# Performance work log

Measured on AMD Instinct MI355X. Metric: run time of the kernel, lower is better.

## Reference

```python
import jax, jax.numpy as jnp
import numpy as np

D_MODEL = 1024
NUM_HEADS = 16
THETA = 10000.0
B, T = 2, 2048


def _rope(x, pos, theta_base):
    # x: (b, h, t, d_h); interleaved pairs (x0,x1),(x2,x3),... per the
    # rearrange '... (c d) -> ... c d' with d=2 in the original module.
    d = x.shape[-1]
    half = d // 2
    inv_freq = 1.0 / (theta_base ** (2.0 * jnp.arange(half, dtype=jnp.float32) / d))
    ang = pos.astype(jnp.float32)[:, None] * inv_freq[None, :]  # (t, half)
    sin = jnp.sin(ang)[None, None]  # (1,1,t,half)
    cos = jnp.cos(ang)[None, None]
    x1 = x[..., 0::2]
    x2 = x[..., 1::2]
    r1 = x1 * cos - x2 * sin
    r2 = x1 * sin + x2 * cos
    return jnp.stack([r1, r2], axis=-1).reshape(x.shape)


def setup_inputs() -> dict:
    key = jax.random.key(0)
    k0, k1, k2, k3, k4 = jax.random.split(key, 5)
    sigma = (2.0 / (D_MODEL + D_MODEL)) ** 0.5
    return {
        "in_features": jax.random.normal(k0, (B, T, D_MODEL), dtype=jnp.float32),
        "Wq": jax.random.normal(k1, (D_MODEL, D_MODEL), dtype=jnp.float32) * sigma,
        "Wk": jax.random.normal(k2, (D_MODEL, D_MODEL), dtype=jnp.float32) * sigma,
        "Wv": jax.random.normal(k3, (D_MODEL, D_MODEL), dtype=jnp.float32) * sigma,
        "Wo": jax.random.normal(k4, (D_MODEL, D_MODEL), dtype=jnp.float32) * sigma,
        "token_positions": jnp.arange(T, dtype=jnp.int32),
    }


def reference(in_features, Wq, Wk, Wv, Wo, token_positions):
    b, t, d_model = in_features.shape
    h = NUM_HEADS
    d_h = d_model // h
    # Fused-style QKV projections (x @ W.T, weights stored (in, out))
    q = in_features @ Wq.T
    k = in_features @ Wk.T
    v = in_features @ Wv.T
    # (b, t, h*d_h) -> (b, h, t, d_h)
    q = q.reshape(b, t, h, d_h).transpose(0, 2, 1, 3)
    k = k.reshape(b, t, h, d_h).transpose(0, 2, 1, 3)
    v = v.reshape(b, t, h, d_h).transpose(0, 2, 1, 3)
    q = _rope(q, token_positions, THETA)
    k = _rope(k, token_positions, THETA)
    scale = 1.0 / jnp.sqrt(jnp.asarray(d_h, dtype=q.dtype))
    scores = jnp.einsum('bhqd,bhkd->bhqk', q, k) * scale
    causal = jnp.tril(jnp.ones((t, t), dtype=bool))
    scores = jnp.where(causal[None, None], scores, -jnp.inf)
    attn = jax.nn.softmax(scores, axis=-1)
    out = jnp.einsum('bhqk,bhkd->bhqd', attn, v)
    out = out.transpose(0, 2, 1, 3).reshape(b, t, h * d_h)
    return out @ Wo.T
```

## Files before the change

kernel.cpp:

```cpp
#include <hip/hip_runtime.h>

#define D_MODEL 1024
#define NUM_HEADS 16
#define DH 64
#define B_SZ 2
#define T_SZ 2048
#define M_ROWS (B_SZ * T_SZ)

typedef __bf16 bf16;
typedef __bf16 bf16x4 __attribute__((ext_vector_type(4)));
typedef __bf16 bf16x8 __attribute__((ext_vector_type(8)));
typedef float f32x4 __attribute__((ext_vector_type(4)));

__device__ __forceinline__ void async_copy16(const bf16* g, bf16* l) {
  __builtin_amdgcn_global_load_lds(
      (const __attribute__((address_space(1))) void*)g,
      (__attribute__((address_space(3))) void*)l, 16, 0, 0);
}

#define NX (M_ROWS * D_MODEL / 4)
#define NW (D_MODEL * D_MODEL / 4)

__global__ __launch_bounds__(256) void cast_all(
    const float* __restrict__ X, const float* __restrict__ Wq,
    const float* __restrict__ Wk, const float* __restrict__ Wv,
    const float* __restrict__ Wo,
    bf16* __restrict__ Xb, bf16* __restrict__ Wqb, bf16* __restrict__ Wkb,
    bf16* __restrict__ Wvb, bf16* __restrict__ Wob) {
  int i = blockIdx.x * 256 + threadIdx.x;
  const float* s; bf16* d; int off;
  if (i < NX) {
    s = X; d = Xb; off = i;
  } else {
    int j = i - NX;
    int w = j >> 18;
    off = j & (NW - 1);
    if (w == 0)      { s = Wq; d = Wqb; }
    else if (w == 1) { s = Wk; d = Wkb; }
    else if (w == 2) { s = Wv; d = Wvb; }
    else             { s = Wo; d = Wob; }
  }
  float4 v = ((const float4*)s)[off];
  bf16x4 o;
  o[0] = (bf16)v.x; o[1] = (bf16)v.y; o[2] = (bf16)v.z; o[3] = (bf16)v.w;
  ((bf16x4*)d)[off] = o;
}

__global__ __launch_bounds__(256) void qkv_gemm(
    const bf16* __restrict__ Xb,
    const bf16* __restrict__ Wqb, const bf16* __restrict__ Wkb,
    const bf16* __restrict__ Wvb,
    bf16* __restrict__ Q, bf16* __restrict__ K, bf16* __restrict__ V) {
  __shared__ bf16 As[128 * 32];
  __shared__ bf16 Bs[128 * 32];

  int tid = threadIdx.x;
  int wave = tid >> 6, lane = tid & 63;
  int wm = wave >> 1, wn = wave & 1;
  int l15 = lane & 15, quad = lane >> 4;

  int row0 = blockIdx.x * 128;
  int col0 = blockIdx.y * 128;
  int sel = col0 >> 10;
  int nb = col0 & 1023;
  const bf16* W; bf16* Out;
  if (sel == 0)      { W = Wqb; Out = Q; }
  else if (sel == 1) { W = Wkb; Out = K; }
  else               { W = Wvb; Out = V; }

  int srow = tid >> 2;
  int schunk = tid & 3;
  const bf16* Ag = Xb + (size_t)(row0 + srow) * D_MODEL + schunk * 8;
  const bf16* Bg = W + (size_t)(nb + srow) * D_MODEL + schunk * 8;
  bf16* Al0 = &As[srow * 32 + schunk * 8];
  bf16* Al1 = &As[(srow + 64) * 32 + schunk * 8];
  bf16* Bl0 = &Bs[srow * 32 + schunk * 8];
  bf16* Bl1 = &Bs[(srow + 64) * 32 + schunk * 8];

  f32x4 acc[4][4];
#pragma unroll
  for (int i = 0; i < 4; ++i)
#pragma unroll
    for (int j = 0; j < 4; ++j) acc[i][j] = (f32x4){0.f, 0.f, 0.f, 0.f};

  for (int k0 = 0; k0 < D_MODEL; k0 += 32) {
    async_copy16(Ag + k0, Al0);
    async_copy16(Ag + k0 + (size_t)64 * D_MODEL, Al1);
    async_copy16(Bg + k0, Bl0);
    async_copy16(Bg + k0 + (size_t)64 * D_MODEL, Bl1);
    __syncthreads();

    bf16x8 af[4], bfr[4];
#pragma unroll
    for (int i = 0; i < 4; ++i)
      af[i] = *(const bf16x8*)&As[(wm * 64 + i * 16 + l15) * 32 + quad * 8];
#pragma unroll
    for (int j = 0; j < 4; ++j)
      bfr[j] = *(const bf16x8*)&Bs[(wn * 64 + j * 16 + l15) * 32 + quad * 8];
#pragma unroll
    for (int i = 0; i < 4; ++i)
#pragma unroll
      for (int j = 0; j < 4; ++j)
        acc[i][j] = __builtin_amdgcn_mfma_f32_16x16x32_bf16(af[i], bfr[j],
                                                            acc[i][j], 0, 0, 0);
    __syncthreads();
  }

#pragma unroll
  for (int i = 0; i < 4; ++i) {
    int row = row0 + wm * 64 + i * 16 + quad * 4;
#pragma unroll
    for (int j = 0; j < 4; ++j) {
      int col = nb + wn * 64 + j * 16 + l15;
#pragma unroll
      for (int r = 0; r < 4; ++r)
        Out[(size_t)(row + r) * D_MODEL + col] = (bf16)acc[i][j][r];
    }
  }
}

#define ROPEK_BLOCKS (M_ROWS * NUM_HEADS * 32 / 256)

__global__ __launch_bounds__(256) void ropek_vt(
    bf16* __restrict__ K, const bf16* __restrict__ V, bf16* __restrict__ VT,
    const int* __restrict__ pos) {
  int b0 = blockIdx.x;
  if (b0 < ROPEK_BLOCKS) {
    int idx = b0 * 256 + threadIdx.x;
    int i = idx & 31;
    int h = (idx >> 5) & 15;
    int row = idx >> 9;
    int t = row & (T_SZ - 1);
    float p = (float)pos[t];
    float freq = __expf(-(float)i * 0.28782313662425f);
    float s, c;
    sincosf(p * freq, &s, &c);
    size_t base = (size_t)row * D_MODEL + h * DH + 2 * i;
    float k1 = (float)K[base], k2 = (float)K[base + 1];
    K[base]     = (bf16)(k1 * c - k2 * s);
    K[base + 1] = (bf16)(k1 * s + k2 * c);
  } else {
    __shared__ bf16 tile[64][72];
    int vb = b0 - ROPEK_BLOCKS;
    int bh = vb >> 5;
    int tt = vb & 31;
    int b = bh >> 4, h = bh & 15;
    int tid = threadIdx.x;
    int rr = tid >> 3;
    int cc = (tid & 7) * 8;
#pragma unroll
    for (int p = 0; p < 2; ++p) {
      int t = rr + p * 32;
      bf16x8 v = *(const bf16x8*)&V[((size_t)b * T_SZ + tt * 64 + t) * D_MODEL +
                                    h * DH + cc];
      *(bf16x8*)&tile[t][cc] = v;
    }
    __syncthreads();
#pragma unroll
    for (int p = 0; p < 2; ++p) {
      int d = rr + p * 32;
      bf16x8 o;
#pragma unroll
      for (int j = 0; j < 8; ++j) o[j] = tile[cc + j][d];
      *(bf16x8*)&VT[((size_t)bh * DH + d) * T_SZ + tt * 64 + cc] = o;
    }
  }
}

#define PST 72
#define KST 72

__global__ __launch_bounds__(256) void attn_kernel(
    const bf16* __restrict__ Q, const bf16* __restrict__ K,
    const bf16* __restrict__ VT, const int* __restrict__ pos,
    bf16* __restrict__ AO) {
  __shared__ bf16 Kt[64 * KST];
  __shared__ bf16 Vt[64 * KST];
  __shared__ bf16 Pbuf[4][16 * PST];

  int bh = blockIdx.x;
  int qi = 31 - (int)blockIdx.y;
  int bb = bh >> 4, h = bh & 15;
  int tid = threadIdx.x;
  int wave = tid >> 6, lane = tid & 63;
  int l15 = lane & 15, quad = lane >> 4;

  int q0 = qi * 64 + wave * 16;
  size_t grow = (size_t)bb * T_SZ + q0;

  const bf16* Qp = Q + (grow + l15) * D_MODEL + h * DH + quad * 8;
  bf16x8 bq0 = *(const bf16x8*)(Qp);
  bf16x8 bq1 = *(const bf16x8*)(Qp + 32);
  {
    float p = (float)pos[q0 + l15];
#pragma unroll
    for (int jj = 0; jj < 4; ++jj) {
      int i0 = quad * 4 + jj;
      float s, c;
      sincosf(p * __expf(-(float)i0 * 0.28782313662425f), &s, &c);
      float x1 = (float)bq0[2 * jj], x2 = (float)bq0[2 * jj + 1];
      bq0[2 * jj]     = (bf16)(x1 * c - x2 * s);
      bq0[2 * jj + 1] = (bf16)(x1 * s + x2 * c);
      sincosf(p * __expf(-(float)(i0 + 16) * 0.28782313662425f), &s, &c);
      float y1 = (float)bq1[2 * jj], y2 = (float)bq1[2 * jj + 1];
      bq1[2 * jj]     = (bf16)(y1 * c - y2 * s);
      bq1[2 * jj + 1] = (bf16)(y1 * s + y2 * c);
    }
  }

  f32x4 o[4];
#pragma unroll
  for (int nt = 0; nt < 4; ++nt) o[nt] = (f32x4){0.f, 0.f, 0.f, 0.f};
  float l_i = 0.f;

  int srow = tid >> 2;
  int sc = (tid & 3) * 16;
  const bf16* Kg = K + ((size_t)bb * T_SZ + srow) * D_MODEL + h * DH + sc;
  const bf16* Vg = VT + ((size_t)bh * DH + srow) * T_SZ + sc;
  bf16* Kl = &Kt[srow * KST + sc];
  bf16* Vl = &Vt[srow * KST + sc];

  bf16* Pw = Pbuf[wave];
  int nchunks = qi + 1;
  int rel = wave * 16 + l15;

  bf16x8 kr0 = *(const bf16x8*)(Kg);
  bf16x8 kr1 = *(const bf16x8*)(Kg + 8);
  bf16x8 vr0 = *(const bf16x8*)(Vg);
  bf16x8 vr1 = *(const bf16x8*)(Vg + 8);

  for (int t = 0; t < nchunks; ++t) {
    __syncthreads();
    *(bf16x8*)(Kl) = kr0;
    *(bf16x8*)(Kl + 8) = kr1;
    *(bf16x8*)(Vl) = vr0;
    *(bf16x8*)(Vl + 8) = vr1;
    if (t + 1 < nchunks) {
      const bf16* Kn = Kg + (size_t)(t + 1) * 64 * D_MODEL;
      const bf16* Vn = Vg + (t + 1) * 64;
      kr0 = *(const bf16x8*)(Kn);
      kr1 = *(const bf16x8*)(Kn + 8);
      vr0 = *(const bf16x8*)(Vn);
      vr1 = *(const bf16x8*)(Vn + 8);
    }
    __syncthreads();

    f32x4 st[4];
#pragma unroll
    for (int cs = 0; cs < 4; ++cs) {
      bf16x8 ak0 = *(const bf16x8*)&Kt[(cs * 16 + l15) * KST + quad * 8];
      bf16x8 ak1 = *(const bf16x8*)&Kt[(cs * 16 + l15) * KST + 32 + quad * 8];
      f32x4 s4 = (f32x4){0.f, 0.f, 0.f, 0.f};
      s4 = __builtin_amdgcn_mfma_f32_16x16x32_bf16(ak0, bq0, s4, 0, 0, 0);
      s4 = __builtin_amdgcn_mfma_f32_16x16x32_bf16(ak1, bq1, s4, 0, 0, 0);
      st[cs] = s4;
    }

    bool last = (t == nchunks - 1);
    float ps = 0.f;
#pragma unroll
    for (int cs = 0; cs < 4; ++cs)
#pragma unroll
      for (int r = 0; r < 4; ++r) {
        float p = __expf(st[cs][r] * 0.125f);
        if (last) {
          int cl = cs * 16 + quad * 4 + r;
          p = (cl > rel) ? 0.f : p;
        }
        st[cs][r] = p;
        ps += p;
      }
    l_i += ps;

#pragma unroll
    for (int cs = 0; cs < 4; ++cs) {
      bf16x4 pk;
#pragma unroll
      for (int r = 0; r < 4; ++r) pk[r] = (bf16)st[cs][r];
      *(bf16x4*)&Pw[l15 * PST + cs * 16 + quad * 4] = pk;
    }
    __asm__ __volatile__("" ::: "memory");
    bf16x8 bp0 = *(const bf16x8*)&Pw[l15 * PST + quad * 8];
    bf16x8 bp1 = *(const bf16x8*)&Pw[l15 * PST + 32 + quad * 8];
    __asm__ __volatile__("" ::: "memory");

#pragma unroll
    for (int nt = 0; nt < 4; ++nt) {
      bf16x8 av0 = *(const bf16x8*)&Vt[(nt * 16 + l15) * KST + quad * 8];
      bf16x8 av1 = *(const bf16x8*)&Vt[(nt * 16 + l15) * KST + 32 + quad * 8];
      o[nt] = __builtin_amdgcn_mfma_f32_16x16x32_bf16(av0, bp0, o[nt], 0, 0, 0);
      o[nt] = __builtin_amdgcn_mfma_f32_16x16x32_bf16(av1, bp1, o[nt], 0, 0, 0);
    }
  }

  l_i += __shfl_xor(l_i, 16);
  l_i += __shfl_xor(l_i, 32);
  float inv = 1.0f / l_i;
#pragma unroll
  for (int nt = 0; nt < 4; ++nt) {
    bf16x4 ov;
#pragma unroll
    for (int r = 0; r < 4; ++r) ov[r] = (bf16)(o[nt][r] * inv);
    *(bf16x4*)&AO[(grow + l15) * D_MODEL + h * DH + nt * 16 + quad * 4] = ov;
  }
}

__global__ __launch_bounds__(256) void out_gemm(
    const bf16* __restrict__ AO, const bf16* __restrict__ Wob,
    float* __restrict__ out) {
  __shared__ bf16 As[128 * 32];
  __shared__ bf16 Bs[64 * 32];

  int tid = threadIdx.x;
  int wave = tid >> 6, lane = tid & 63;
  int l15 = lane & 15, quad = lane >> 4;

  int row0 = blockIdx.x * 128;
  int nb = blockIdx.y * 64;

  int srow = tid >> 2;
  int schunk = tid & 3;
  const bf16* Ag = AO + (size_t)(row0 + srow) * D_MODEL + schunk * 8;
  const bf16* Bg = Wob + (size_t)(nb + srow) * D_MODEL + schunk * 8;
  bf16* Al0 = &As[srow * 32 + schunk * 8];
  bf16* Al1 = &As[(srow + 64) * 32 + schunk * 8];
  bf16* Bl = &Bs[srow * 32 + schunk * 8];

  f32x4 acc[2][4];
#pragma unroll
  for (int i = 0; i < 2; ++i)
#pragma unroll
    for (int j = 0; j < 4; ++j) acc[i][j] = (f32x4){0.f, 0.f, 0.f, 0.f};

  for (int k0 = 0; k0 < D_MODEL; k0 += 32) {
    async_copy16(Ag + k0, Al0);
    async_copy16(Ag + k0 + (size_t)64 * D_MODEL, Al1);
    async_copy16(Bg + k0, Bl);
    __syncthreads();

    bf16x8 af[2], bfr[4];
#pragma unroll
    for (int i = 0; i < 2; ++i)
      af[i] = *(const bf16x8*)&As[(wave * 32 + i * 16 + l15) * 32 + quad * 8];
#pragma unroll
    for (int j = 0; j < 4; ++j)
      bfr[j] = *(const bf16x8*)&Bs[(j * 16 + l15) * 32 + quad * 8];
#pragma unroll
    for (int i = 0; i < 2; ++i)
#pragma unroll
      for (int j = 0; j < 4; ++j)
        acc[i][j] = __builtin_amdgcn_mfma_f32_16x16x32_bf16(af[i], bfr[j],
                                                            acc[i][j], 0, 0, 0);
    __syncthreads();
  }

#pragma unroll
  for (int i = 0; i < 2; ++i) {
    int row = row0 + wave * 32 + i * 16 + quad * 4;
#pragma unroll
    for (int j = 0; j < 4; ++j) {
      int col = nb + j * 16 + l15;
#pragma unroll
      for (int r = 0; r < 4; ++r)
        out[(size_t)(row + r) * D_MODEL + col] = acc[i][j][r];
    }
  }
}

extern "C" void kernel_launch(void* const* d_in, const int* in_sizes, int n_in,
                              void* d_out, int out_size, void* d_ws, size_t ws_size,
                              hipStream_t stream) {
  const float* X  = (const float*)d_in[0];
  const float* Wq = (const float*)d_in[1];
  const float* Wk = (const float*)d_in[2];
  const float* Wv = (const float*)d_in[3];
  const float* Wo = (const float*)d_in[4];
  const int*  pos = (const int*)d_in[5];
  float* out = (float*)d_out;

  char* w = (char*)d_ws;
  bf16* Xb  = (bf16*)w;  w += (size_t)M_ROWS * D_MODEL * 2;
  bf16* Wqb = (bf16*)w;  w += (size_t)D_MODEL * D_MODEL * 2;
  bf16* Wkb = (bf16*)w;  w += (size_t)D_MODEL * D_MODEL * 2;
  bf16* Wvb = (bf16*)w;  w += (size_t)D_MODEL * D_MODEL * 2;
  bf16* Wob = (bf16*)w;  w += (size_t)D_MODEL * D_MODEL * 2;
  bf16* Qb  = (bf16*)w;  w += (size_t)M_ROWS * D_MODEL * 2;
  bf16* Kb  = (bf16*)w;  w += (size_t)M_ROWS * D_MODEL * 2;
  bf16* Vb  = (bf16*)w;  w += (size_t)M_ROWS * D_MODEL * 2;
  bf16* AO  = (bf16*)w;  w += (size_t)M_ROWS * D_MODEL * 2;
  bf16* VT  = (bf16*)w;  w += (size_t)M_ROWS * D_MODEL * 2;

  cast_all<<<(NX + 4 * NW) / 256, 256, 0, stream>>>(X, Wq, Wk, Wv, Wo,
                                                    Xb, Wqb, Wkb, Wvb, Wob);
  qkv_gemm<<<dim3(M_ROWS / 128, 3 * D_MODEL / 128), 256, 0, stream>>>(
      Xb, Wqb, Wkb, Wvb, Qb, Kb, Vb);
  ropek_vt<<<ROPEK_BLOCKS + B_SZ * NUM_HEADS * (T_SZ / 64), 256, 0, stream>>>(
      Kb, Vb, VT, pos);
  attn_kernel<<<dim3(B_SZ * NUM_HEADS, T_SZ / 64), 256, 0, stream>>>(
      Qb, Kb, VT, pos, AO);
  out_gemm<<<dim3(M_ROWS / 128, D_MODEL / 64), 256, 0, stream>>>(AO, Wob, out);
}
```

Baseline: 185.6 us.

## Split attention keys across waves with cross-wave reduction of partial outputs

The attention kernel now has each wave cover all 64 query rows of the block, but only a 32-key slice of a 128-key chunk, instead of one 16-row query slice over all keys. Each wave keeps 16 output accumulators in registers. At the end the partial outputs and row sums of the four waves are reduced through LDS, and the causal diagonal lets whole waves skip the last chunk. Register loading of K/V tiles with prefetch is replaced by loading at the start of each iteration, with larger tiles and new padding strides. This cuts the number of chunk iterations and barriers and reuses each K/V fragment across four query tiles, at the cost of more register pressure, an LDS reduction epilogue, and no prefetch overlap.

```diff
diff --git a/kernel.cpp b/kernel.cpp
--- a/kernel.cpp
+++ b/kernel.cpp
@@ -167,16 +167,18 @@
   }
 }
 
-#define PST 72
-#define KST 72
-
-__global__ __launch_bounds__(256) void attn_kernel(
+#define KST 68
+#define VST 132
+#define PSTW 34
+
+__global__ __launch_bounds__(256, 2) void attn_kernel(
     const bf16* __restrict__ Q, const bf16* __restrict__ K,
     const bf16* __restrict__ VT, const int* __restrict__ pos,
     bf16* __restrict__ AO) {
-  __shared__ bf16 Kt[64 * KST];
-  __shared__ bf16 Vt[64 * KST];
-  __shared__ bf16 Pbuf[4][16 * PST];
+  __shared__ bf16 Kt[128 * KST];
+  __shared__ bf16 Vt[64 * VST];
+  __shared__ bf16 Pb[4][64 * PSTW];
+  __shared__ float lbuf[4][64];
 
   int bh = blockIdx.x;
   int qi = 31 - (int)blockIdx.y;
@@ -185,124 +187,190 @@
   int wave = tid >> 6, lane = tid & 63;
   int l15 = lane & 15, quad = lane >> 4;
 
-  int q0 = qi * 64 + wave * 16;
-  size_t grow = (size_t)bb * T_SZ + q0;
-
-  const bf16* Qp = Q + (grow + l15) * D_MODEL + h * DH + quad * 8;
-  bf16x8 bq0 = *(const bf16x8*)(Qp);
-  bf16x8 bq1 = *(const bf16x8*)(Qp + 32);
-  {
-    float p = (float)pos[q0 + l15];
+  size_t qrowbase = (size_t)bb * T_SZ + qi * 64;
+
+  bf16x8 bq[4][2];
+#pragma unroll
+  for (int qs = 0; qs < 4; ++qs) {
+    const bf16* Qp = Q + (qrowbase + qs * 16 + l15) * D_MODEL + h * DH + quad * 8;
+    bq[qs][0] = *(const bf16x8*)(Qp);
+    bq[qs][1] = *(const bf16x8*)(Qp + 32);
+    float p = (float)pos[qi * 64 + qs * 16 + l15];
 #pragma unroll
     for (int jj = 0; jj < 4; ++jj) {
       int i0 = quad * 4 + jj;
       float s, c;
       sincosf(p * __expf(-(float)i0 * 0.28782313662425f), &s, &c);
-      float x1 = (float)bq0[2 * jj], x2 = (float)bq0[2 * jj + 1];
-      bq0[2 * jj]     = (bf16)(x1 * c - x2 * s);
-      bq0[2 * jj + 1] = (bf16)(x1 * s + x2 * c);
+      float x1 = (float)bq[qs][0][2 * jj], x2 = (float)bq[qs][0][2 * jj + 1];
+      bq[qs][0][2 * jj]     = (bf16)(x1 * c - x2 * s);
+      bq[qs][0][2 * jj + 1] = (bf16)(x1 * s + x2 * c);
       sincosf(p * __expf(-(float)(i0 + 16) * 0.28782313662425f), &s, &c);
-      float y1 = (float)bq1[2 * jj], y2 = (float)bq1[2 * jj + 1];
-      bq1[2 * jj]     = (bf16)(y1 * c - y2 * s);
-      bq1[2 * jj + 1] = (bf16)(y1 * s + y2 * c);
-    }
-  }
-
-  f32x4 o[4];
-#pragma unroll
-  for (int nt = 0; nt < 4; ++nt) o[nt] = (f32x4){0.f, 0.f, 0.f, 0.f};
-  float l_i = 0.f;
-
-  int srow = tid >> 2;
-  int sc = (tid & 3) * 16;
-  const bf16* Kg = K + ((size_t)bb * T_SZ + srow) * D_MODEL + h * DH + sc;
-  const bf16* Vg = VT + ((size_t)bh * DH + srow) * T_SZ + sc;
-  bf16* Kl = &Kt[srow * KST + sc];
-  bf16* Vl = &Vt[srow * KST + sc];
-
-  bf16* Pw = Pbuf[wave];
-  int nchunks = qi + 1;
-  int rel = wave * 16 + l15;
-
-  bf16x8 kr0 = *(const bf16x8*)(Kg);
-  bf16x8 kr1 = *(const bf16x8*)(Kg + 8);
-  bf16x8 vr0 = *(const bf16x8*)(Vg);
-  bf16x8 vr1 = *(const bf16x8*)(Vg + 8);
+      float y1 = (float)bq[qs][1][2 * jj], y2 = (float)bq[qs][1][2 * jj + 1];
+      bq[qs][1][2 * jj]     = (bf16)(y1 * c - y2 * s);
+      bq[qs][1][2 * jj + 1] = (bf16)(y1 * s + y2 * c);
+    }
+  }
+
+  f32x4 o[4][4];
+#pragma unroll
+  for (int nt = 0; nt < 4; ++nt)
+#pragma unroll
+    for (int qs = 0; qs < 4; ++qs) o[nt][qs] = (f32x4){0.f, 0.f, 0.f, 0.f};
+  float lp[4] = {0.f, 0.f, 0.f, 0.f};
+
+  int ksrow = tid >> 1;
+  int kcol = (tid & 1) * 32;
+  const bf16* Kg = K + ((size_t)bb * T_SZ + ksrow) * D_MODEL + h * DH + kcol;
+  bf16* Klp = &Kt[ksrow * KST + kcol];
+  int vdrow = tid >> 2;
+  int vcol = (tid & 3) * 32;
+  const bf16* Vg = VT + ((size_t)bh * DH + vdrow) * T_SZ + vcol;
+  bf16* Vlp = &Vt[vdrow * VST + vcol];
+
+  bf16* Pw = Pb[wave];
+  int nchunks = (qi + 2) >> 1;
+  int cw = wave * 32;
 
   for (int t = 0; t < nchunks; ++t) {
-    __syncthreads();
-    *(bf16x8*)(Kl) = kr0;
-    *(bf16x8*)(Kl + 8) = kr1;
-    *(bf16x8*)(Vl) = vr0;
-    *(bf16x8*)(Vl + 8) = vr1;
-    if (t + 1 < nchunks) {
-      const bf16* Kn = Kg + (size_t)(t + 1) * 64 * D_MODEL;
-      const bf16* Vn = Vg + (t + 1) * 64;
-      kr0 = *(const bf16x8*)(Kn);
-      kr1 = *(const bf16x8*)(Kn + 8);
-      vr0 = *(const bf16x8*)(Vn);
-      vr1 = *(const bf16x8*)(Vn + 8);
-    }
-    __syncthreads();
-
-    f32x4 st[4];
-#pragma unroll
-    for (int cs = 0; cs < 4; ++cs) {
-      bf16x8 ak0 = *(const bf16x8*)&Kt[(cs * 16 + l15) * KST + quad * 8];
-      bf16x8 ak1 = *(const bf16x8*)&Kt[(cs * 16 + l15) * KST + 32 + quad * 8];
-      f32x4 s4 = (f32x4){0.f, 0.f, 0.f, 0.f};
-      s4 = __builtin_amdgcn_mfma_f32_16x16x32_bf16(ak0, bq0, s4, 0, 0, 0);
-      s4 = __builtin_amdgcn_mfma_f32_16x16x32_bf16(ak1, bq1, s4, 0, 0, 0);
-      st[cs] = s4;
-    }
-
-    bool last = (t == nchunks - 1);
-    float ps = 0.f;
-#pragma unroll
-    for (int cs = 0; cs < 4; ++cs)
-#pragma unroll
-      for (int r = 0; r < 4; ++r) {
-        float p = __expf(st[cs][r] * 0.125f);
-        if (last) {
-          int cl = cs * 16 + quad * 4 + r;
-          p = (cl > rel) ? 0.f : p;
+    const bf16* Ks = Kg + (size_t)t * 128 * D_MODEL;
+    const bf16* Vs = Vg + t * 128;
+    bf16x8 kr[4], vr[4];
+#pragma unroll
+    for (int m = 0; m < 4; ++m) kr[m] = *(const bf16x8*)(Ks + m * 8);
+#pragma unroll
+    for (int m = 0; m < 4; ++m) vr[m] = *(const bf16x8*)(Vs + m * 8);
+    __syncthreads();
+#pragma unroll
+    for (int m = 0; m < 4; ++m) *(bf16x8*)(Klp + m * 8) = kr[m];
+#pragma unroll
+    for (int m = 0; m < 4; ++m) *(bf16x8*)(Vlp + m * 8) = vr[m];
+    __syncthreads();
+
+    bool lastc = (t == nchunks - 1);
+    bool wactive = !lastc || (128 * t + cw <= 64 * qi + 63);
+    if (wactive) {
+      f32x4 st[2][4];
+#pragma unroll
+      for (int cs = 0; cs < 2; ++cs) {
+        const bf16* kb = &Kt[(cw + cs * 16 + l15) * KST + quad * 8];
+        bf16x8 ak0 = *(const bf16x8*)(kb);
+        bf16x8 ak1 = *(const bf16x8*)(kb + 32);
+#pragma unroll
+        for (int qs = 0; qs < 4; ++qs) {
+          f32x4 s4 = (f32x4){0.f, 0.f, 0.f, 0.f};
+          s4 = __builtin_amdgcn_mfma_f32_16x16x32_bf16(ak0, bq[qs][0], s4, 0, 0, 0);
+          s4 = __builtin_amdgcn_mfma_f32_16x16x32_bf16(ak1, bq[qs][1], s4, 0, 0, 0);
+          st[cs][qs] = s4;
         }
-        st[cs][r] = p;
-        ps += p;
       }
-    l_i += ps;
-
-#pragma unroll
-    for (int cs = 0; cs < 4; ++cs) {
-      bf16x4 pk;
-#pragma unroll
-      for (int r = 0; r < 4; ++r) pk[r] = (bf16)st[cs][r];
-      *(bf16x4*)&Pw[l15 * PST + cs * 16 + quad * 4] = pk;
-    }
-    __asm__ __volatile__("" ::: "memory");
-    bf16x8 bp0 = *(const bf16x8*)&Pw[l15 * PST + quad * 8];
-    bf16x8 bp1 = *(const bf16x8*)&Pw[l15 * PST + 32 + quad * 8];
-    __asm__ __volatile__("" ::: "memory");
-
-#pragma unroll
-    for (int nt = 0; nt < 4; ++nt) {
-      bf16x8 av0 = *(const bf16x8*)&Vt[(nt * 16 + l15) * KST + quad * 8];
-      bf16x8 av1 = *(const bf16x8*)&Vt[(nt * 16 + l15) * KST + 32 + quad * 8];
-      o[nt] = __builtin_amdgcn_mfma_f32_16x16x32_bf16(av0, bp0, o[nt], 0, 0, 0);
-      o[nt] = __builtin_amdgcn_mfma_f32_16x16x32_bf16(av1, bp1, o[nt], 0, 0, 0);
-    }
-  }
-
-  l_i += __shfl_xor(l_i, 16);
-  l_i += __shfl_xor(l_i, 32);
-  float inv = 1.0f / l_i;
-#pragma unroll
-  for (int nt = 0; nt < 4; ++nt) {
-    bf16x4 ov;
-#pragma unroll
-    for (int r = 0; r < 4; ++r) ov[r] = (bf16)(o[nt][r] * inv);
-    *(bf16x4*)&AO[(grow + l15) * D_MODEL + h * DH + nt * 16 + quad * 4] = ov;
-  }
+
+      int cb = 128 * t + cw;
+#pragma unroll
+      for (int cs = 0; cs < 2; ++cs)
+#pragma unroll
+        for (int qs = 0; qs < 4; ++qs) {
+          bf16x4 pk;
+#pragma unroll
+          for (int r = 0; r < 4; ++r) {
+            float pv = __expf(st[cs][qs][r] * 0.125f);
+            if (lastc) {
+              int cl = cb + cs * 16 + quad * 4 + r;
+              int ql = 64 * qi + qs * 16 + l15;
+              pv = (cl > ql) ? 0.f : pv;
+            }
+            lp[qs] += pv;
+            pk[r] = (bf16)pv;
+          }
+          *(bf16x4*)&Pw[(qs * 16 + l15) * PSTW + cs * 16 + quad * 4] = pk;
+        }
+      __asm__ __volatile__("" ::: "memory");
+
+      bf16x8 av[4];
+#pragma unroll
+      for (int nt = 0; nt < 4; ++nt)
+        av[nt] = *(const bf16x8*)&Vt[(nt * 16 + l15) * VST + cw + quad * 8];
+#pragma unroll
+      for (int qs = 0; qs < 4; ++qs) {
+        bf16x8 bp = *(const bf16x8*)&Pw[(qs * 16 + l15) * PSTW + quad * 8];
+#pragma unroll
+        for (int nt = 0; nt < 4; ++nt)
+          o[nt][qs] = __builtin_amdgcn_mfma_f32_16x16x32_bf16(av[nt], bp,
+                                                              o[nt][qs], 0, 0, 0);
+      }
+      __asm__ __volatile__("" ::: "memory");
+    }
+  }
+
+#pragma unroll
+  for (int qs = 0; qs < 4; ++qs) {
+    lp[qs] += __shfl_xor(lp[qs], 16);
+    lp[qs] += __shfl_xor(lp[qs], 32);
+    if (quad == 0) lbuf[wave][qs * 16 + l15] = lp[qs];
+  }
+  __syncthreads();
+
+  float* MA = (float*)Kt;
+  float* MB = (float*)Pb;
+#define MIDX(qs, nt) (((qs) * 16 + l15) * 68 + (nt) * 16 + quad * 4)
+  if (wave == 1) {
+#pragma unroll
+    for (int nt = 0; nt < 4; ++nt)
+#pragma unroll
+      for (int qs = 0; qs < 4; ++qs) *(f32x4*)&MA[MIDX(qs, nt)] = o[nt][qs];
+  } else if (wave == 3) {
+#pragma unroll
+    for (int nt = 0; nt < 4; ++nt)
+#pragma unroll
+      for (int qs = 0; qs < 4; ++qs) *(f32x4*)&MB[MIDX(qs, nt)] = o[nt][qs];
+  }
+  __syncthreads();
+  if (wave == 0) {
+#pragma unroll
+    for (int nt = 0; nt < 4; ++nt)
+#pragma unroll
+      for (int qs = 0; qs < 4; ++qs) {
+        f32x4 v = *(const f32x4*)&MA[MIDX(qs, nt)];
+#pragma unroll
+        for (int r = 0; r < 4; ++r) o[nt][qs][r] += v[r];
+      }
+  } else if (wave == 2) {
+#pragma unroll
+    for (int nt = 0; nt < 4; ++nt)
+#pragma unroll
+      for (int qs = 0; qs < 4; ++qs) {
+        f32x4 v = *(const f32x4*)&MB[MIDX(qs, nt)];
+#pragma unroll
+        for (int r = 0; r < 4; ++r) o[nt][qs][r] += v[r];
+      }
+  }
+  __syncthreads();
+  if (wave == 2) {
+#pragma unroll
+    for (int nt = 0; nt < 4; ++nt)
+#pragma unroll
+      for (int qs = 0; qs < 4; ++qs) *(f32x4*)&MA[MIDX(qs, nt)] = o[nt][qs];
+  }
+  __syncthreads();
+  if (wave == 0) {
+    float linv[4];
+#pragma unroll
+    for (int qs = 0; qs < 4; ++qs)
+      linv[qs] = 1.0f / (lbuf[0][qs * 16 + l15] + lbuf[1][qs * 16 + l15] +
+                         lbuf[2][qs * 16 + l15] + lbuf[3][qs * 16 + l15]);
+#pragma unroll
+    for (int nt = 0; nt < 4; ++nt)
+#pragma unroll
+      for (int qs = 0; qs < 4; ++qs) {
+        f32x4 v = *(const f32x4*)&MA[MIDX(qs, nt)];
+        bf16x4 ov;
+#pragma unroll
+        for (int r = 0; r < 4; ++r)
+          ov[r] = (bf16)((o[nt][qs][r] + v[r]) * linv[qs]);
+        *(bf16x4*)&AO[(qrowbase + qs * 16 + l15) * D_MODEL + h * DH +
+                      nt * 16 + quad * 4] = ov;
+      }
+  }
+#undef MIDX
 }
 
 __global__ __launch_bounds__(256) void out_gemm(
```

Measured after the change: 258.4 us. 39.2% more time.

## Fuse fp32-to-bf16 casts, K RoPE and V transpose into GEMM kernels

Applied to the files above, without the earlier changes.

Removes the separate cast kernel and the RoPE-K/V-transpose kernel. The QKV GEMM now loads fp32 inputs and weights directly, converts them to bf16 in registers with a one-step register prefetch, and applies RoPE to K (using a lane shuffle for the pair partner) and writes V transposed in its epilogue. The output GEMM likewise converts fp32 Wo on the fly. This cuts two launches and the bf16 intermediate round trips, but it doubles global bytes per GEMM tile load, replaces async LDS copies with synchronous register staging, and recomputes weight casts in every block that reads them.

```diff
diff --git a/kernel.cpp b/kernel.cpp
--- a/kernel.cpp
+++ b/kernel.cpp
@@ -18,39 +18,18 @@
       (__attribute__((address_space(3))) void*)l, 16, 0, 0);
 }
 
-#define NX (M_ROWS * D_MODEL / 4)
-#define NW (D_MODEL * D_MODEL / 4)
-
-__global__ __launch_bounds__(256) void cast_all(
-    const float* __restrict__ X, const float* __restrict__ Wq,
-    const float* __restrict__ Wk, const float* __restrict__ Wv,
-    const float* __restrict__ Wo,
-    bf16* __restrict__ Xb, bf16* __restrict__ Wqb, bf16* __restrict__ Wkb,
-    bf16* __restrict__ Wvb, bf16* __restrict__ Wob) {
-  int i = blockIdx.x * 256 + threadIdx.x;
-  const float* s; bf16* d; int off;
-  if (i < NX) {
-    s = X; d = Xb; off = i;
-  } else {
-    int j = i - NX;
-    int w = j >> 18;
-    off = j & (NW - 1);
-    if (w == 0)      { s = Wq; d = Wqb; }
-    else if (w == 1) { s = Wk; d = Wkb; }
-    else if (w == 2) { s = Wv; d = Wvb; }
-    else             { s = Wo; d = Wob; }
-  }
-  float4 v = ((const float4*)s)[off];
-  bf16x4 o;
-  o[0] = (bf16)v.x; o[1] = (bf16)v.y; o[2] = (bf16)v.z; o[3] = (bf16)v.w;
-  ((bf16x4*)d)[off] = o;
+__device__ __forceinline__ bf16x8 pack8(float4 a, float4 b) {
+  bf16x8 o;
+  o[0] = (bf16)a.x; o[1] = (bf16)a.y; o[2] = (bf16)a.z; o[3] = (bf16)a.w;
+  o[4] = (bf16)b.x; o[5] = (bf16)b.y; o[6] = (bf16)b.z; o[7] = (bf16)b.w;
+  return o;
 }
 
 __global__ __launch_bounds__(256) void qkv_gemm(
-    const bf16* __restrict__ Xb,
-    const bf16* __restrict__ Wqb, const bf16* __restrict__ Wkb,
-    const bf16* __restrict__ Wvb,
-    bf16* __restrict__ Q, bf16* __restrict__ K, bf16* __restrict__ V) {
+    const float* __restrict__ X,
+    const float* __restrict__ Wq, const float* __restrict__ Wk,
+    const float* __restrict__ Wv, const int* __restrict__ pos,
+    bf16* __restrict__ Q, bf16* __restrict__ K, bf16* __restrict__ VT) {
   __shared__ bf16 As[128 * 32];
   __shared__ bf16 Bs[128 * 32];
 
@@ -63,19 +42,16 @@
   int col0 = blockIdx.y * 128;
   int sel = col0 >> 10;
   int nb = col0 & 1023;
-  const bf16* W; bf16* Out;
-  if (sel == 0)      { W = Wqb; Out = Q; }
-  else if (sel == 1) { W = Wkb; Out = K; }
-  else               { W = Wvb; Out = V; }
+  const float* W32 = (sel == 0) ? Wq : (sel == 1) ? Wk : Wv;
 
   int srow = tid >> 2;
-  int schunk = tid & 3;
-  const bf16* Ag = Xb + (size_t)(row0 + srow) * D_MODEL + schunk * 8;
-  const bf16* Bg = W + (size_t)(nb + srow) * D_MODEL + schunk * 8;
-  bf16* Al0 = &As[srow * 32 + schunk * 8];
-  bf16* Al1 = &As[(srow + 64) * 32 + schunk * 8];
-  bf16* Bl0 = &Bs[srow * 32 + schunk * 8];
-  bf16* Bl1 = &Bs[(srow + 64) * 32 + schunk * 8];
+  int sc8 = (tid & 3) * 8;
+  const float* Ag = X + (size_t)(row0 + srow) * D_MODEL + sc8;
+  const float* Bg = W32 + (size_t)(nb + srow) * D_MODEL + sc8;
+  bf16* Al0 = &As[srow * 32 + sc8];
+  bf16* Al1 = &As[(srow + 64) * 32 + sc8];
+  bf16* Bl0 = &Bs[srow * 32 + sc8];
+  bf16* Bl1 = &Bs[(srow + 64) * 32 + sc8];
 
   f32x4 acc[4][4];
 #pragma unroll
@@ -83,11 +59,31 @@
 #pragma unroll
     for (int j = 0; j < 4; ++j) acc[i][j] = (f32x4){0.f, 0.f, 0.f, 0.f};
 
+  float4 a00 = *(const float4*)(Ag);
+  float4 a01 = *(const float4*)(Ag + 4);
+  float4 a10 = *(const float4*)(Ag + (size_t)64 * D_MODEL);
+  float4 a11 = *(const float4*)(Ag + (size_t)64 * D_MODEL + 4);
+  float4 b00 = *(const float4*)(Bg);
+  float4 b01 = *(const float4*)(Bg + 4);
+  float4 b10 = *(const float4*)(Bg + (size_t)64 * D_MODEL);
+  float4 b11 = *(const float4*)(Bg + (size_t)64 * D_MODEL + 4);
+
   for (int k0 = 0; k0 < D_MODEL; k0 += 32) {
-    async_copy16(Ag + k0, Al0);
-    async_copy16(Ag + k0 + (size_t)64 * D_MODEL, Al1);
-    async_copy16(Bg + k0, Bl0);
-    async_copy16(Bg + k0 + (size_t)64 * D_MODEL, Bl1);
+    *(bf16x8*)Al0 = pack8(a00, a01);
+    *(bf16x8*)Al1 = pack8(a10, a11);
+    *(bf16x8*)Bl0 = pack8(b00, b01);
+    *(bf16x8*)Bl1 = pack8(b10, b11);
+    if (k0 + 32 < D_MODEL) {
+      int kn = k0 + 32;
+      a00 = *(const float4*)(Ag + kn);
+      a01 = *(const float4*)(Ag + kn + 4);
+      a10 = *(const float4*)(Ag + (size_t)64 * D_MODEL + kn);
+      a11 = *(const float4*)(Ag + (size_t)64 * D_MODEL + kn + 4);
+      b00 = *(const float4*)(Bg + kn);
+      b01 = *(const float4*)(Bg + kn + 4);
+      b10 = *(const float4*)(Bg + (size_t)64 * D_MODEL + kn);
+      b11 = *(const float4*)(Bg + (size_t)64 * D_MODEL + kn + 4);
+    }
     __syncthreads();
 
     bf16x8 af[4], bfr[4];
@@ -106,63 +102,54 @@
     __syncthreads();
   }
 
-#pragma unroll
-  for (int i = 0; i < 4; ++i) {
-    int row = row0 + wm * 64 + i * 16 + quad * 4;
+  if (sel == 0) {
+#pragma unroll
+    for (int i = 0; i < 4; ++i) {
+      int row = row0 + wm * 64 + i * 16 + quad * 4;
+#pragma unroll
+      for (int j = 0; j < 4; ++j) {
+        int col = nb + wn * 64 + j * 16 + l15;
+#pragma unroll
+        for (int r = 0; r < 4; ++r)
+          Q[(size_t)(row + r) * D_MODEL + col] = (bf16)acc[i][j][r];
+      }
+    }
+  } else if (sel == 1) {
 #pragma unroll
     for (int j = 0; j < 4; ++j) {
       int col = nb + wn * 64 + j * 16 + l15;
-#pragma unroll
-      for (int r = 0; r < 4; ++r)
-        Out[(size_t)(row + r) * D_MODEL + col] = (bf16)acc[i][j][r];
-    }
-  }
-}
-
-#define ROPEK_BLOCKS (M_ROWS * NUM_HEADS * 32 / 256)
-
-__global__ __launch_bounds__(256) void ropek_vt(
-    bf16* __restrict__ K, const bf16* __restrict__ V, bf16* __restrict__ VT,
-    const int* __restrict__ pos) {
-  int b0 = blockIdx.x;
-  if (b0 < ROPEK_BLOCKS) {
-    int idx = b0 * 256 + threadIdx.x;
-    int i = idx & 31;
-    int h = (idx >> 5) & 15;
-    int row = idx >> 9;
-    int t = row & (T_SZ - 1);
-    float p = (float)pos[t];
-    float freq = __expf(-(float)i * 0.28782313662425f);
-    float s, c;
-    sincosf(p * freq, &s, &c);
-    size_t base = (size_t)row * D_MODEL + h * DH + 2 * i;
-    float k1 = (float)K[base], k2 = (float)K[base + 1];
-    K[base]     = (bf16)(k1 * c - k2 * s);
-    K[base + 1] = (bf16)(k1 * s + k2 * c);
+      int ip = (col & 63) >> 1;
+      float freq = __expf(-(float)ip * 0.28782313662425f);
+      bool evenc = (col & 1) == 0;
+#pragma unroll
+      for (int i = 0; i < 4; ++i) {
+        int row = row0 + wm * 64 + i * 16 + quad * 4;
+#pragma unroll
+        for (int r = 0; r < 4; ++r) {
+          float v = acc[i][j][r];
+          float part = __shfl_xor(v, 1);
+          float p = (float)pos[(row + r) & (T_SZ - 1)];
+          float s, c;
+          sincosf(p * freq, &s, &c);
+          float ov = evenc ? (v * c - part * s) : (part * s + v * c);
+          K[(size_t)(row + r) * D_MODEL + col] = (bf16)ov;
+        }
+      }
+    }
   } else {
-    __shared__ bf16 tile[64][72];
-    int vb = b0 - ROPEK_BLOCKS;
-    int bh = vb >> 5;
-    int tt = vb & 31;
-    int b = bh >> 4, h = bh & 15;
-    int tid = threadIdx.x;
-    int rr = tid >> 3;
-    int cc = (tid & 7) * 8;
-#pragma unroll
-    for (int p = 0; p < 2; ++p) {
-      int t = rr + p * 32;
-      bf16x8 v = *(const bf16x8*)&V[((size_t)b * T_SZ + tt * 64 + t) * D_MODEL +
-                                    h * DH + cc];
-      *(bf16x8*)&tile[t][cc] = v;
-    }
-    __syncthreads();
-#pragma unroll
-    for (int p = 0; p < 2; ++p) {
-      int d = rr + p * 32;
-      bf16x8 o;
-#pragma unroll
-      for (int j = 0; j < 8; ++j) o[j] = tile[cc + j][d];
-      *(bf16x8*)&VT[((size_t)bh * DH + d) * T_SZ + tt * 64 + cc] = o;
+    int b = row0 >> 11;
+#pragma unroll
+    for (int j = 0; j < 4; ++j) {
+      int col = nb + wn * 64 + j * 16 + l15;
+      size_t vbase = ((size_t)(b * 16 + (col >> 6)) * 64 + (col & 63)) * T_SZ;
+#pragma unroll
+      for (int i = 0; i < 4; ++i) {
+        int t0 = (row0 & (T_SZ - 1)) + wm * 64 + i * 16 + quad * 4;
+        bf16x4 ov;
+#pragma unroll
+        for (int r = 0; r < 4; ++r) ov[r] = (bf16)acc[i][j][r];
+        *(bf16x4*)&VT[vbase + t0] = ov;
+      }
     }
   }
 }
@@ -306,7 +293,7 @@
 }
 
 __global__ __launch_bounds__(256) void out_gemm(
-    const bf16* __restrict__ AO, const bf16* __restrict__ Wob,
+    const bf16* __restrict__ AO, const float* __restrict__ Wo,
     float* __restrict__ out) {
   __shared__ bf16 As[128 * 32];
   __shared__ bf16 Bs[64 * 32];
@@ -319,23 +306,30 @@
   int nb = blockIdx.y * 64;
 
   int srow = tid >> 2;
-  int schunk = tid & 3;
-  const bf16* Ag = AO + (size_t)(row0 + srow) * D_MODEL + schunk * 8;
-  const bf16* Bg = Wob + (size_t)(nb + srow) * D_MODEL + schunk * 8;
-  bf16* Al0 = &As[srow * 32 + schunk * 8];
-  bf16* Al1 = &As[(srow + 64) * 32 + schunk * 8];
-  bf16* Bl = &Bs[srow * 32 + schunk * 8];
+  int sc8 = (tid & 3) * 8;
+  const bf16* Ag = AO + (size_t)(row0 + srow) * D_MODEL + sc8;
+  const float* Bg = Wo + (size_t)(nb + srow) * D_MODEL + sc8;
+  bf16* Al0 = &As[srow * 32 + sc8];
+  bf16* Al1 = &As[(srow + 64) * 32 + sc8];
+  bf16* Bl = &Bs[srow * 32 + sc8];
 
   f32x4 acc[2][4];
 #pragma unroll
   for (int i = 0; i < 2; ++i)
 #pragma unroll
     for (int j = 0; j < 4; ++j) acc[i][j] = (f32x4){0.f, 0.f, 0.f, 0.f};
+
+  float4 wb0 = *(const float4*)(Bg);
+  float4 wb1 = *(const float4*)(Bg + 4);
 
   for (int k0 = 0; k0 < D_MODEL; k0 += 32) {
     async_copy16(Ag + k0, Al0);
     async_copy16(Ag + k0 + (size_t)64 * D_MODEL, Al1);
-    async_copy16(Bg + k0, Bl);
+    *(bf16x8*)Bl = pack8(wb0, wb1);
+    if (k0 + 32 < D_MODEL) {
+      wb0 = *(const float4*)(Bg + k0 + 32);
+      wb1 = *(const float4*)(Bg + k0 + 36);
+    }
     __syncthreads();
 
     bf16x8 af[2], bfr[4];
@@ -379,24 +373,14 @@
   float* out = (float*)d_out;
 
   char* w = (char*)d_ws;
-  bf16* Xb  = (bf16*)w;  w += (size_t)M_ROWS * D_MODEL * 2;
-  bf16* Wqb = (bf16*)w;  w += (size_t)D_MODEL * D_MODEL * 2;
-  bf16* Wkb = (bf16*)w;  w += (size_t)D_MODEL * D_MODEL * 2;
-  bf16* Wvb = (bf16*)w;  w += (size_t)D_MODEL * D_MODEL * 2;
-  bf16* Wob = (bf16*)w;  w += (size_t)D_MODEL * D_MODEL * 2;
-  bf16* Qb  = (bf16*)w;  w += (size_t)M_ROWS * D_MODEL * 2;
-  bf16* Kb  = (bf16*)w;  w += (size_t)M_ROWS * D_MODEL * 2;
-  bf16* Vb  = (bf16*)w;  w += (size_t)M_ROWS * D_MODEL * 2;
-  bf16* AO  = (bf16*)w;  w += (size_t)M_ROWS * D_MODEL * 2;
-  bf16* VT  = (bf16*)w;  w += (size_t)M_ROWS * D_MODEL * 2;
-
-  cast_all<<<(NX + 4 * NW) / 256, 256, 0, stream>>>(X, Wq, Wk, Wv, Wo,
-                                                    Xb, Wqb, Wkb, Wvb, Wob);
+  bf16* Qb = (bf16*)w;  w += (size_t)M_ROWS * D_MODEL * 2;
+  bf16* Kb = (bf16*)w;  w += (size_t)M_ROWS * D_MODEL * 2;
+  bf16* VT = (bf16*)w;  w += (size_t)M_ROWS * D_MODEL * 2;
+  bf16* AO = (bf16*)w;  w += (size_t)M_ROWS * D_MODEL * 2;
+
   qkv_gemm<<<dim3(M_ROWS / 128, 3 * D_MODEL / 128), 256, 0, stream>>>(
-      Xb, Wqb, Wkb, Wvb, Qb, Kb, Vb);
-  ropek_vt<<<ROPEK_BLOCKS + B_SZ * NUM_HEADS * (T_SZ / 64), 256, 0, stream>>>(
-      Kb, Vb, VT, pos);
+      X, Wq, Wk, Wv, pos, Qb, Kb, VT);
   attn_kernel<<<dim3(B_SZ * NUM_HEADS, T_SZ / 64), 256, 0, stream>>>(
       Qb, Kb, VT, pos, AO);
-  out_gemm<<<dim3(M_ROWS / 128, D_MODEL / 64), 256, 0, stream>>>(AO, Wob, out);
-}
+  out_gemm<<<dim3(M_ROWS / 128, D_MODEL / 64), 256, 0, stream>>>(AO, Wo, out);
+}
```

New measurement: 430.0 us. +131.8%, slower.
